# Performance work log

Hardware: AMD Instinct MI355X
Metric: run time of the kernel (lower is better)

Reference implementation:

```python
import jax, jax.numpy as jnp
import numpy as np

SOS_TOKEN = 0
VOCAB, EMBED, HIDDEN = 32000, 256, 256


def setup_inputs() -> dict:
    key = jax.random.key(0)
    ks = jax.random.split(key, 10)
    B, S, T = 32, 128, 128
    s = 0.05
    return {
        "encoder_outputs": jax.random.normal(ks[0], (B, S, HIDDEN), jnp.float32),
        "encoder_hidden": jax.random.normal(ks[1], (1, B, HIDDEN), jnp.float32),
        "target_tensor": jax.random.randint(ks[2], (B, T), 0, VOCAB),
        "embedding": jax.random.normal(ks[3], (VOCAB, EMBED), jnp.float32) * s,
        "W_ih": jax.random.normal(ks[4], (3 * HIDDEN, EMBED + HIDDEN), jnp.float32) * s,
        "W_hh": jax.random.normal(ks[5], (3 * HIDDEN, HIDDEN), jnp.float32) * s,
        "b_ih": jax.random.normal(ks[6], (3 * HIDDEN,), jnp.float32) * s,
        "b_hh": jax.random.normal(ks[7], (3 * HIDDEN,), jnp.float32) * s,
        "W_out": jax.random.normal(ks[8], (VOCAB, HIDDEN), jnp.float32) * s,
        "b_out": jax.random.normal(ks[9], (VOCAB,), jnp.float32) * s,
    }


def _decode(encoder_outputs, encoder_hidden, target_tensor, embedding,
            W_ih, W_hh, b_ih, b_hh, W_out, b_out):
    B, T = target_tensor.shape
    # full teacher forcing: decoder input at step t is target[t-1], step 0 is SOS
    dec_in = jnp.concatenate(
        [jnp.full((B, 1), SOS_TOKEN, dtype=target_tensor.dtype), target_tensor[:, :-1]], axis=1)
    emb = embedding[dec_in]                                     # (B,T,E)
    # attention: query = embedded input, key = value = encoder_outputs
    scores = jnp.einsum("bte,bse->bts", emb, encoder_outputs)   # (B,T,S)
    attn = jax.nn.softmax(scores, axis=2)
    context = jnp.einsum("bts,bsh->bth", attn, encoder_outputs)  # (B,T,H)
    x_seq = jnp.concatenate([emb, context], axis=2)             # (B,T,E+H)
    x_seq = jnp.swapaxes(x_seq, 0, 1)                           # (T,B,E+H)

    def gru_step(h, x):
        gi = x @ W_ih.T + b_ih                                  # (B,3H)
        gh = h @ W_hh.T + b_hh
        i_r, i_z, i_n = jnp.split(gi, 3, axis=1)
        h_r, h_z, h_n = jnp.split(gh, 3, axis=1)
        r = jax.nn.sigmoid(i_r + h_r)
        z = jax.nn.sigmoid(i_z + h_z)
        n = jnp.tanh(i_n + r * h_n)
        h_new = (1.0 - z) * n + z * h
        return h_new, h_new

    h0 = encoder_hidden[0]                                      # (B,H)
    _, hs = jax.lax.scan(gru_step, h0, x_seq)                   # (T,B,H)
    logits = hs @ W_out.T + b_out                               # (T,B,V)
    return jnp.swapaxes(logits, 0, 1)                           # (B,T,V)


def reference(encoder_outputs, encoder_hidden, target_tensor, embedding,
              W_ih, W_hh, b_ih, b_hh, W_out, b_out):
    return _decode(encoder_outputs, encoder_hidden, target_tensor, embedding,
                   W_ih, W_hh, b_ih, b_hh, W_out, b_out)
```

## Files before the change

kernel.cpp:

```cpp
#include <hip/hip_runtime.h>
#include <hip/hip_bf16.h>
#include <stdint.h>

typedef float  f32x4  __attribute__((ext_vector_type(4)));
typedef __bf16 bf16x8 __attribute__((ext_vector_type(8)));
typedef _Float16 h2v  __attribute__((ext_vector_type(2)));

#define B_ 32
#define S_ 128
#define T_ 128
#define H_ 256
#define E_ 256
#define V_ 32000

__device__ __forceinline__ void gll16(const void* g, void* l) {
  __builtin_amdgcn_global_load_lds(
      (const __attribute__((address_space(1))) uint32_t*)g,
      (__attribute__((address_space(3))) uint32_t*)l,
      16, 0, 0);
}

__device__ __forceinline__ uint32_t pack_pair(float a, float b) {
  unsigned short lo = __builtin_bit_cast(unsigned short, (_Float16)a);
  unsigned short hi = __builtin_bit_cast(unsigned short, (_Float16)b);
  return (uint32_t)lo | ((uint32_t)hi << 16);
}

__device__ __forceinline__ float dot2(uint32_t w, uint32_t h, float acc) {
#if __has_builtin(__builtin_amdgcn_fdot2)
  return __builtin_amdgcn_fdot2(__builtin_bit_cast(h2v, w),
                                __builtin_bit_cast(h2v, h), acc, false);
#else
  h2v wv = __builtin_bit_cast(h2v, w);
  h2v hv = __builtin_bit_cast(h2v, h);
  return acc + (float)wv.x * (float)hv.x + (float)wv.y * (float)hv.y;
#endif
}

__global__ __launch_bounds__(256) void cvt_bf16_kernel(
    const float* __restrict__ src, __hip_bfloat16* __restrict__ dst, int n) {
  int i = (blockIdx.x * 256 + threadIdx.x) * 4;
  if (i + 3 < n) {
    float4 v = *(const float4*)(src + i);
    dst[i + 0] = __float2bfloat16(v.x);
    dst[i + 1] = __float2bfloat16(v.y);
    dst[i + 2] = __float2bfloat16(v.z);
    dst[i + 3] = __float2bfloat16(v.w);
  }
}

__global__ __launch_bounds__(256) void pack_whh(
    const float* __restrict__ Whh, uint32_t* __restrict__ Wp) {
  __shared__ float lds[32][257];
  int j0 = blockIdx.x * 32;
  int tid = threadIdx.x;
  #pragma unroll 4
  for (int i = 0; i < 32; ++i)
    lds[i][tid] = Whh[(size_t)(j0 + i) * 256 + tid];
  __syncthreads();
  #pragma unroll 4
  for (int i = 0; i < 16; ++i) {
    int e = i * 256 + tid;
    int k2 = e >> 5;
    int jj = e & 31;
    Wp[(size_t)k2 * 768 + j0 + jj] = pack_pair(lds[jj][2 * k2], lds[jj][2 * k2 + 1]);
  }
}

__global__ __launch_bounds__(256) void attn_kernel(
    const float* __restrict__ enc,
    const int*   __restrict__ tgt,
    const float* __restrict__ embt,
    float*       __restrict__ x_seq)
{
  int b   = blockIdx.x;
  int tc  = blockIdx.y;
  int tid = threadIdx.x;
  __shared__ __align__(16) float e_sh[256];
  __shared__ float attn_sh[128];
  __shared__ float red_sh[4];
  const float* encb = enc + (size_t)b * S_ * H_;

  for (int tt = 0; tt < 8; ++tt) {
    int t = tc * 8 + tt;
    int tok = (t == 0) ? 0 : tgt[b * T_ + t - 1];
    float ev = embt[(size_t)tok * E_ + tid];
    e_sh[tid] = ev;
    x_seq[(size_t)(t * B_ + b) * 512 + tid] = ev;
    __syncthreads();

    float sc = 0.f;
    if (tid < 128) {
      const float* er = encb + tid * H_;
      #pragma unroll 8
      for (int k = 0; k < 256; k += 4) {
        float4 e4 = *(const float4*)(e_sh + k);
        float4 r4 = *(const float4*)(er + k);
        sc += e4.x * r4.x; sc += e4.y * r4.y; sc += e4.z * r4.z; sc += e4.w * r4.w;
      }
      float mx = sc;
      #pragma unroll
      for (int o = 32; o > 0; o >>= 1) mx = fmaxf(mx, __shfl_xor(mx, o, 64));
      if ((tid & 63) == 0) red_sh[tid >> 6] = mx;
    }
    __syncthreads();
    float gmax = fmaxf(red_sh[0], red_sh[1]);
    float p = 0.f;
    if (tid < 128) {
      p = expf(sc - gmax);
      float s = p;
      #pragma unroll
      for (int o = 32; o > 0; o >>= 1) s += __shfl_xor(s, o, 64);
      if ((tid & 63) == 0) red_sh[2 + (tid >> 6)] = s;
    }
    __syncthreads();
    float tot = red_sh[2] + red_sh[3];
    if (tid < 128) attn_sh[tid] = p / tot;
    __syncthreads();

    float ctx = 0.f;
    #pragma unroll 4
    for (int s = 0; s < 128; ++s) ctx += attn_sh[s] * encb[s * H_ + tid];
    x_seq[(size_t)(t * B_ + b) * 512 + 256 + tid] = ctx;
    __syncthreads();
  }
}

__global__ __launch_bounds__(256) void gi_gemm(
    const float* __restrict__ X,
    const float* __restrict__ W,
    const float* __restrict__ bih,
    float*       __restrict__ gi)
{
  __shared__ float As[64][17];
  __shared__ float Bs[64][17];
  int tid = threadIdx.x;
  int n0 = blockIdx.x * 64;
  int m0 = blockIdx.y * 64;
  int tx = tid & 15, ty = tid >> 4;
  int lr = tid >> 2, lc = (tid & 3) * 4;
  float acc[16] = {};

  for (int k0 = 0; k0 < 512; k0 += 16) {
    float4 a4 = *(const float4*)(X + (size_t)(m0 + lr) * 512 + k0 + lc);
    float4 b4 = *(const float4*)(W + (size_t)(n0 + lr) * 512 + k0 + lc);
    As[lr][lc + 0] = a4.x; As[lr][lc + 1] = a4.y; As[lr][lc + 2] = a4.z; As[lr][lc + 3] = a4.w;
    Bs[lr][lc + 0] = b4.x; Bs[lr][lc + 1] = b4.y; Bs[lr][lc + 2] = b4.z; Bs[lr][lc + 3] = b4.w;
    __syncthreads();
    #pragma unroll
    for (int kk = 0; kk < 16; ++kk) {
      float ar[4], br[4];
      #pragma unroll
      for (int i = 0; i < 4; ++i) ar[i] = As[ty * 4 + i][kk];
      #pragma unroll
      for (int j = 0; j < 4; ++j) br[j] = Bs[tx * 4 + j][kk];
      #pragma unroll
      for (int i = 0; i < 4; ++i)
        #pragma unroll
        for (int j = 0; j < 4; ++j)
          acc[i * 4 + j] += ar[i] * br[j];
    }
    __syncthreads();
  }
  #pragma unroll
  for (int i = 0; i < 4; ++i) {
    int m = m0 + ty * 4 + i;
    #pragma unroll
    for (int j = 0; j < 4; ++j) {
      int n = n0 + tx * 4 + j;
      gi[(size_t)m * 768 + n] = acc[i * 4 + j] + bih[n];
    }
  }
}

__global__ __launch_bounds__(768) void gru_kernel(
    const float*    __restrict__ gi,
    const uint32_t* __restrict__ Wp,
    const float*    __restrict__ bhh,
    const float*    __restrict__ h0,
    __hip_bfloat16* __restrict__ hs)
{
  int b   = blockIdx.x;
  int tid = threadIdx.x;
  int role = tid >> 8;
  int j    = tid & 255;
  __shared__ __align__(16) uint32_t h2[128];
  __shared__ float r_sh[256];
  __shared__ float z_sh[256];

  uint32_t w[128];
  #pragma unroll
  for (int i = 0; i < 128; ++i) w[i] = Wp[(size_t)i * 768 + tid];
  float bj = bhh[tid];

  float hprev = 0.f;
  if (role == 2) {
    hprev = h0[b * 256 + j];
    float other = __shfl_xor(hprev, 1);
    if (!(j & 1)) h2[j >> 1] = pack_pair(hprev, other);
  }
  float gval = gi[(size_t)b * 768 + tid];
  __syncthreads();

  for (int t = 0; t < 128; ++t) {
    float gnext = 0.f;
    if (t < 127) gnext = gi[(size_t)((t + 1) * 32 + b) * 768 + tid];

    float a0 = 0.f, a1 = 0.f, a2 = 0.f, a3 = 0.f;
    float a4 = 0.f, a5 = 0.f, a6 = 0.f, a7 = 0.f;
    #pragma unroll
    for (int k8 = 0; k8 < 16; ++k8) {
      uint4 ha = *(const uint4*)&h2[k8 * 8];
      uint4 hb = *(const uint4*)&h2[k8 * 8 + 4];
      a0 = dot2(w[k8 * 8 + 0], ha.x, a0);
      a1 = dot2(w[k8 * 8 + 1], ha.y, a1);
      a2 = dot2(w[k8 * 8 + 2], ha.z, a2);
      a3 = dot2(w[k8 * 8 + 3], ha.w, a3);
      a4 = dot2(w[k8 * 8 + 4], hb.x, a4);
      a5 = dot2(w[k8 * 8 + 5], hb.y, a5);
      a6 = dot2(w[k8 * 8 + 6], hb.z, a6);
      a7 = dot2(w[k8 * 8 + 7], hb.w, a7);
    }
    float gh = ((a0 + a1) + (a2 + a3)) + ((a4 + a5) + (a6 + a7)) + bj;

    if (role == 0)      r_sh[j] = 1.f / (1.f + expf(-(gval + gh)));
    else if (role == 1) z_sh[j] = 1.f / (1.f + expf(-(gval + gh)));
    __syncthreads();

    if (role == 2) {
      float r = r_sh[j];
      float z = z_sh[j];
      float n = tanhf(gval + r * gh);
      float hn = (1.f - z) * n + z * hprev;
      hprev = hn;
      hs[(size_t)(t * 32 + b) * 256 + j] = __float2bfloat16(hn);
      float other = __shfl_xor(hn, 1);
      if (!(j & 1)) h2[j >> 1] = pack_pair(hn, other);
    }
    gval = gnext;
    __syncthreads();
  }
}

__global__ __launch_bounds__(256) void logits_gemm(
    const __hip_bfloat16* __restrict__ A,
    const __hip_bfloat16* __restrict__ Bm,
    const float* __restrict__ bout,
    float* __restrict__ out)
{
  __shared__ __hip_bfloat16 sA[128 * 64];
  __shared__ __hip_bfloat16 sB[128 * 64];
  int tid = threadIdx.x;
  int n0 = blockIdx.x * 128;
  int m0 = blockIdx.y * 128;
  int lane = tid & 63;
  int wave = tid >> 6;
  int wm = (wave >> 1) * 64;
  int wn = (wave & 1) * 64;
  int srow = tid >> 3;
  int sk   = (tid & 7) * 8;
  f32x4 acc[4][4] = {};

  for (int kt = 0; kt < 256; kt += 64) {
    #pragma unroll
    for (int it = 0; it < 4; ++it) {
      int row = it * 32 + srow;
      gll16(A  + (size_t)(m0 + row) * 256 + kt + sk, &sA[row * 64 + sk]);
      gll16(Bm + (size_t)(n0 + row) * 256 + kt + sk, &sB[row * 64 + sk]);
    }
    __syncthreads();
    #pragma unroll
    for (int kk = 0; kk < 2; ++kk) {
      bf16x8 af[4], bfr[4];
      #pragma unroll
      for (int m = 0; m < 4; ++m)
        af[m] = *(const bf16x8*)&sA[(wm + m * 16 + (lane & 15)) * 64 + kk * 32 + (lane >> 4) * 8];
      #pragma unroll
      for (int n = 0; n < 4; ++n)
        bfr[n] = *(const bf16x8*)&sB[(wn + n * 16 + (lane & 15)) * 64 + kk * 32 + (lane >> 4) * 8];
      #pragma unroll
      for (int m = 0; m < 4; ++m)
        #pragma unroll
        for (int n = 0; n < 4; ++n)
          acc[m][n] = __builtin_amdgcn_mfma_f32_16x16x32_bf16(af[m], bfr[n], acc[m][n], 0, 0, 0);
    }
    __syncthreads();
  }

  #pragma unroll
  for (int n = 0; n < 4; ++n) {
    int col = n0 + wn + n * 16 + (lane & 15);
    float bv = bout[col];
    #pragma unroll
    for (int m = 0; m < 4; ++m) {
      int rbase = m0 + wm + m * 16 + (lane >> 4) * 4;
      #pragma unroll
      for (int r = 0; r < 4; ++r) {
        int row = rbase + r;
        int t  = row >> 5;
        int bb = row & 31;
        out[(size_t)(bb * 128 + t) * 32000 + col] = acc[m][n][r] + bv;
      }
    }
  }
}

extern "C" void kernel_launch(void* const* d_in, const int* in_sizes, int n_in,
                              void* d_out, int out_size, void* d_ws, size_t ws_size,
                              hipStream_t stream) {
  const float* enc  = (const float*)d_in[0];
  const float* ench = (const float*)d_in[1];
  const int*   tgt  = (const int*)d_in[2];
  const float* embt = (const float*)d_in[3];
  const float* Wih  = (const float*)d_in[4];
  const float* Whh  = (const float*)d_in[5];
  const float* bih  = (const float*)d_in[6];
  const float* bhh  = (const float*)d_in[7];
  const float* Wout = (const float*)d_in[8];
  const float* bout = (const float*)d_in[9];
  float* out = (float*)d_out;

  char* ws = (char*)d_ws;
  float* x_seq = (float*)(ws);
  float* gi    = (float*)(ws + 8388608);
  __hip_bfloat16* hs    = (__hip_bfloat16*)(ws + 20971520);
  __hip_bfloat16* woutb = (__hip_bfloat16*)(ws + 23068672);

  uint32_t* Wp = (uint32_t*)(out + ((size_t)out_size - 98304));

  cvt_bf16_kernel<<<8000, 256, 0, stream>>>(Wout, woutb, V_ * H_);
  pack_whh<<<24, 256, 0, stream>>>(Whh, Wp);
  attn_kernel<<<dim3(32, 16), 256, 0, stream>>>(enc, tgt, embt, x_seq);
  gi_gemm<<<dim3(12, 64), 256, 0, stream>>>(x_seq, Wih, bih, gi);
  gru_kernel<<<32, 768, 0, stream>>>(gi, Wp, bhh, ench, hs);
  logits_gemm<<<dim3(250, 32), 256, 0, stream>>>(hs, woutb, bout, out);
}
```

Measured before the change: 549.9 us.

## Use f16 MFMA for input-gate GEMM and swizzle logits GEMM block order

Attention now writes the GRU input sequence as packed fp16 instead of fp32, and W_ih is converted to fp16. The scalar fp32 tiled gi GEMM is replaced by an MFMA 16x16x32 f16 kernel that loads through global_load_lds. Separately, the logits GEMM launch becomes a 1D grid with a remapped block order that groups M tiles into chunks, aiming for better L2 reuse of the weight tiles. Casting the inputs to fp16 reduces precision and adds a small conversion kernel.

```diff
diff --git a/kernel.cpp b/kernel.cpp
--- a/kernel.cpp
+++ b/kernel.cpp
@@ -2,9 +2,10 @@
 #include <hip/hip_bf16.h>
 #include <stdint.h>
 
-typedef float  f32x4  __attribute__((ext_vector_type(4)));
-typedef __bf16 bf16x8 __attribute__((ext_vector_type(8)));
-typedef _Float16 h2v  __attribute__((ext_vector_type(2)));
+typedef float    f32x4  __attribute__((ext_vector_type(4)));
+typedef __bf16   bf16x8 __attribute__((ext_vector_type(8)));
+typedef _Float16 f16x8  __attribute__((ext_vector_type(8)));
+typedef _Float16 h2v    __attribute__((ext_vector_type(2)));
 
 #define B_ 32
 #define S_ 128
@@ -46,6 +47,18 @@
     dst[i + 1] = __float2bfloat16(v.y);
     dst[i + 2] = __float2bfloat16(v.z);
     dst[i + 3] = __float2bfloat16(v.w);
+  }
+}
+
+__global__ __launch_bounds__(256) void cvt_f16_kernel(
+    const float* __restrict__ src, uint32_t* __restrict__ dst, int n) {
+  int i = (blockIdx.x * 256 + threadIdx.x) * 4;
+  if (i + 3 < n) {
+    float4 v = *(const float4*)(src + i);
+    uint2 p;
+    p.x = pack_pair(v.x, v.y);
+    p.y = pack_pair(v.z, v.w);
+    *(uint2*)(dst + (i >> 1)) = p;
   }
 }
 
@@ -71,7 +84,7 @@
     const float* __restrict__ enc,
     const int*   __restrict__ tgt,
     const float* __restrict__ embt,
-    float*       __restrict__ x_seq)
+    uint32_t*    __restrict__ xh)
 {
   int b   = blockIdx.x;
   int tc  = blockIdx.y;
@@ -86,7 +99,11 @@
     int tok = (t == 0) ? 0 : tgt[b * T_ + t - 1];
     float ev = embt[(size_t)tok * E_ + tid];
     e_sh[tid] = ev;
-    x_seq[(size_t)(t * B_ + b) * 512 + tid] = ev;
+    {
+      float other = __shfl_xor(ev, 1);
+      if (!(tid & 1))
+        xh[(size_t)(t * B_ + b) * 256 + (tid >> 1)] = pack_pair(ev, other);
+    }
     __syncthreads();
 
     float sc = 0.f;
@@ -121,54 +138,70 @@
     float ctx = 0.f;
     #pragma unroll 4
     for (int s = 0; s < 128; ++s) ctx += attn_sh[s] * encb[s * H_ + tid];
-    x_seq[(size_t)(t * B_ + b) * 512 + 256 + tid] = ctx;
-    __syncthreads();
-  }
-}
-
-__global__ __launch_bounds__(256) void gi_gemm(
-    const float* __restrict__ X,
-    const float* __restrict__ W,
+    {
+      float other = __shfl_xor(ctx, 1);
+      if (!(tid & 1))
+        xh[(size_t)(t * B_ + b) * 256 + 128 + (tid >> 1)] = pack_pair(ctx, other);
+    }
+    __syncthreads();
+  }
+}
+
+__global__ __launch_bounds__(256) void gi_gemm_f16(
+    const _Float16* __restrict__ A,
+    const _Float16* __restrict__ Bm,
     const float* __restrict__ bih,
-    float*       __restrict__ gi)
+    float* __restrict__ gi)
 {
-  __shared__ float As[64][17];
-  __shared__ float Bs[64][17];
-  int tid = threadIdx.x;
-  int n0 = blockIdx.x * 64;
-  int m0 = blockIdx.y * 64;
-  int tx = tid & 15, ty = tid >> 4;
-  int lr = tid >> 2, lc = (tid & 3) * 4;
-  float acc[16] = {};
-
-  for (int k0 = 0; k0 < 512; k0 += 16) {
-    float4 a4 = *(const float4*)(X + (size_t)(m0 + lr) * 512 + k0 + lc);
-    float4 b4 = *(const float4*)(W + (size_t)(n0 + lr) * 512 + k0 + lc);
-    As[lr][lc + 0] = a4.x; As[lr][lc + 1] = a4.y; As[lr][lc + 2] = a4.z; As[lr][lc + 3] = a4.w;
-    Bs[lr][lc + 0] = b4.x; Bs[lr][lc + 1] = b4.y; Bs[lr][lc + 2] = b4.z; Bs[lr][lc + 3] = b4.w;
-    __syncthreads();
-    #pragma unroll
-    for (int kk = 0; kk < 16; ++kk) {
-      float ar[4], br[4];
-      #pragma unroll
-      for (int i = 0; i < 4; ++i) ar[i] = As[ty * 4 + i][kk];
-      #pragma unroll
-      for (int j = 0; j < 4; ++j) br[j] = Bs[tx * 4 + j][kk];
-      #pragma unroll
-      for (int i = 0; i < 4; ++i)
+  __shared__ _Float16 sA[128 * 64];
+  __shared__ _Float16 sB[128 * 64];
+  int tid = threadIdx.x;
+  int n0 = blockIdx.x * 128;
+  int m0 = blockIdx.y * 128;
+  int lane = tid & 63;
+  int wave = tid >> 6;
+  int wm = (wave >> 1) * 64;
+  int wn = (wave & 1) * 64;
+  int srow = tid >> 3;
+  int sk   = (tid & 7) * 8;
+  f32x4 acc[4][4] = {};
+
+  for (int kt = 0; kt < 512; kt += 64) {
+    #pragma unroll
+    for (int it = 0; it < 4; ++it) {
+      int row = it * 32 + srow;
+      gll16(A  + (size_t)(m0 + row) * 512 + kt + sk, &sA[row * 64 + sk]);
+      gll16(Bm + (size_t)(n0 + row) * 512 + kt + sk, &sB[row * 64 + sk]);
+    }
+    __syncthreads();
+    #pragma unroll
+    for (int kk = 0; kk < 2; ++kk) {
+      f16x8 af[4], bfr[4];
+      #pragma unroll
+      for (int m = 0; m < 4; ++m)
+        af[m] = *(const f16x8*)&sA[(wm + m * 16 + (lane & 15)) * 64 + kk * 32 + (lane >> 4) * 8];
+      #pragma unroll
+      for (int n = 0; n < 4; ++n)
+        bfr[n] = *(const f16x8*)&sB[(wn + n * 16 + (lane & 15)) * 64 + kk * 32 + (lane >> 4) * 8];
+      #pragma unroll
+      for (int m = 0; m < 4; ++m)
         #pragma unroll
-        for (int j = 0; j < 4; ++j)
-          acc[i * 4 + j] += ar[i] * br[j];
-    }
-    __syncthreads();
-  }
+        for (int n = 0; n < 4; ++n)
+          acc[m][n] = __builtin_amdgcn_mfma_f32_16x16x32_f16(af[m], bfr[n], acc[m][n], 0, 0, 0);
+    }
+    __syncthreads();
+  }
+
   #pragma unroll
-  for (int i = 0; i < 4; ++i) {
-    int m = m0 + ty * 4 + i;
-    #pragma unroll
-    for (int j = 0; j < 4; ++j) {
-      int n = n0 + tx * 4 + j;
-      gi[(size_t)m * 768 + n] = acc[i * 4 + j] + bih[n];
+  for (int n = 0; n < 4; ++n) {
+    int col = n0 + wn + n * 16 + (lane & 15);
+    float bv = bih[col];
+    #pragma unroll
+    for (int m = 0; m < 4; ++m) {
+      int rbase = m0 + wm + m * 16 + (lane >> 4) * 4;
+      #pragma unroll
+      for (int r = 0; r < 4; ++r)
+        gi[(size_t)(rbase + r) * 768 + col] = acc[m][n][r] + bv;
     }
   }
 }
@@ -251,8 +284,11 @@
   __shared__ __hip_bfloat16 sA[128 * 64];
   __shared__ __hip_bfloat16 sB[128 * 64];
   int tid = threadIdx.x;
-  int n0 = blockIdx.x * 128;
-  int m0 = blockIdx.y * 128;
+  int bid = blockIdx.x;
+  int chunk = bid & 7;
+  int local = bid >> 3;
+  int m0 = (chunk * 4 + (local & 3)) * 128;
+  int n0 = (local >> 2) * 128;
   int lane = tid & 63;
   int wave = tid >> 6;
   int wm = (wave >> 1) * 64;
@@ -321,17 +357,19 @@
   float* out = (float*)d_out;
 
   char* ws = (char*)d_ws;
-  float* x_seq = (float*)(ws);
-  float* gi    = (float*)(ws + 8388608);
-  __hip_bfloat16* hs    = (__hip_bfloat16*)(ws + 20971520);
-  __hip_bfloat16* woutb = (__hip_bfloat16*)(ws + 23068672);
+  float*          gi    = (float*)(ws);
+  __hip_bfloat16* hs    = (__hip_bfloat16*)(ws + 12582912);
+  __hip_bfloat16* woutb = (__hip_bfloat16*)(ws + 14680064);
+  uint32_t*       xh    = (uint32_t*)(ws + 31064064);
+  uint32_t*       wihh  = (uint32_t*)(ws + 35258368);
 
   uint32_t* Wp = (uint32_t*)(out + ((size_t)out_size - 98304));
 
   cvt_bf16_kernel<<<8000, 256, 0, stream>>>(Wout, woutb, V_ * H_);
+  cvt_f16_kernel<<<384, 256, 0, stream>>>(Wih, wihh, 768 * 512);
   pack_whh<<<24, 256, 0, stream>>>(Whh, Wp);
-  attn_kernel<<<dim3(32, 16), 256, 0, stream>>>(enc, tgt, embt, x_seq);
-  gi_gemm<<<dim3(12, 64), 256, 0, stream>>>(x_seq, Wih, bih, gi);
+  attn_kernel<<<dim3(32, 16), 256, 0, stream>>>(enc, tgt, embt, xh);
+  gi_gemm_f16<<<dim3(6, 32), 256, 0, stream>>>((const _Float16*)xh, (const _Float16*)wihh, bih, gi);
   gru_kernel<<<32, 768, 0, stream>>>(gi, Wp, bhh, ench, hs);
-  logits_gemm<<<dim3(250, 32), 256, 0, stream>>>(hs, woutb, bout, out);
-}
+  logits_gemm<<<8000, 256, 0, stream>>>(hs, woutb, bout, out);
+}
```

New measurement: 490.9 us. -10.7%, faster.
